# Optimization experiments

Measured on AMD Instinct MI355X. Metric: run time of the kernel, lower is better.

The kernel has to match this reference:

```python
import jax, jax.numpy as jnp
import numpy as np

EPS_NORM = 1e-12  # F.normalize eps
EPS_LN = 1e-5     # nn.LayerNorm default eps

def _l2norm(x, axis=-1):
    n = jnp.linalg.norm(x, axis=axis, keepdims=True)
    return x / jnp.maximum(n, EPS_NORM)

def setup_inputs() -> dict:
    key = jax.random.key(0)
    k1, k2 = jax.random.split(key)
    n, b, d = 2048, 8, 1024
    x = jax.random.normal(k1, (n, b, d), dtype=jnp.float32)
    embed = jax.random.normal(k2, (n, d), dtype=jnp.float32)  # xavier-like
    gamma = jnp.ones((d,), dtype=jnp.float32)
    beta = jnp.zeros((d,), dtype=jnp.float32)
    return {"x": x, "embed": embed, "gamma": gamma, "beta": beta}

def reference(x, embed, gamma, beta):
    # x: [n, b, d]; embed: [n, d] (broadcast over batch, as in .expand)
    wn = _l2norm(embed)          # [n, d]
    xn = _l2norm(x)              # [n, b, d]
    scores = jnp.einsum('nd,mbd->nbm', wn, xn)    # cosine similarities
    weights = jax.nn.softmax(scores, axis=-1)     # [n, b, m]
    out = jnp.einsum('nbm,mbd->nbd', weights, x)  # weighted sum of raw input
    # dropout is identity in eval mode
    y = out + x
    mu = jnp.mean(y, axis=-1, keepdims=True)
    var = jnp.var(y, axis=-1, keepdims=True)
    return (y - mu) * jax.lax.rsqrt(var + EPS_LN) * gamma + beta
```

## Files before the change

### kernel.cpp

```cpp
#include <hip/hip_runtime.h>
#include <hip/hip_bf16.h>

typedef float f4 __attribute__((ext_vector_type(4)));
typedef int i32x4 __attribute__((ext_vector_type(4)));
typedef int i32x8 __attribute__((ext_vector_type(8)));
typedef unsigned char u8x16 __attribute__((ext_vector_type(16)));
typedef unsigned short u16x8 __attribute__((ext_vector_type(8)));

#define N_TOK 2048
#define BATCH 8
#define DIM   1024

#if defined(__has_builtin)
#if __has_builtin(__builtin_amdgcn_cvt_scalef32_pk_fp4_f32)
#define HAS_FP4_CVT 1
#endif
#endif

static __device__ __forceinline__ unsigned char fp8_1(float a) {
  return (unsigned char)(__builtin_amdgcn_cvt_pk_fp8_f32(a, a, 0, false) & 0xFF);
}
static __device__ __forceinline__ unsigned short f2bf(float f) {
  unsigned int b = __float_as_uint(f);
  b += 0x7FFFu + ((b >> 16) & 1u);
  return (unsigned short)(b >> 16);
}
static __device__ __forceinline__ float bf2f(unsigned short u) {
  return __uint_as_float(((unsigned int)u) << 16);
}
static __device__ __forceinline__ unsigned int fp4_enc(float v) {
  const float a = fabsf(v);
  unsigned int c = (a >= 0.25f) + (a >= 0.75f) + (a >= 1.25f) + (a >= 1.75f)
                 + (a >= 2.5f) + (a >= 3.5f) + (a >= 5.0f);
  return c | (v < 0.0f ? 8u : 0u);
}
static __device__ __forceinline__ unsigned int pk8_fp4(const float* v) {
#ifdef HAS_FP4_CVT
  unsigned int r = 0;
  r = __builtin_amdgcn_cvt_scalef32_pk_fp4_f32(r, v[0], v[1], 1.0f, 0);
  r = __builtin_amdgcn_cvt_scalef32_pk_fp4_f32(r, v[2], v[3], 1.0f, 1);
  r = __builtin_amdgcn_cvt_scalef32_pk_fp4_f32(r, v[4], v[5], 1.0f, 2);
  r = __builtin_amdgcn_cvt_scalef32_pk_fp4_f32(r, v[6], v[7], 1.0f, 3);
  return r;
#else
  unsigned int r = 0;
  #pragma unroll
  for (int i = 0; i < 8; ++i) r |= fp4_enc(v[i]) << (i * 4);
  return r;
#endif
}

static __device__ __forceinline__ void gld16(const void* g, void* lds) {
  __builtin_amdgcn_global_load_lds(
      (const __attribute__((address_space(1))) unsigned int*)g,
      (__attribute__((address_space(3))) unsigned int*)lds, 16, 0, 0);
}

static __device__ __forceinline__ void stage_tile(const unsigned char* g, size_t ldb,
                                                  unsigned char* lds, int w, int l) {
  const int rgrp = l >> 3;
  const int srcb = (((l & 7) ^ rgrp) << 4);
  #pragma unroll
  for (int gi = 0; gi < 4; ++gi) {
    int rb = (gi * 4 + w) * 8;
    gld16(g + (size_t)(rb + rgrp) * ldb + srcb, lds + (gi * 4 + w) * 1024);
  }
}

static __device__ __forceinline__ i32x8 fragld32(const unsigned char* lds, int row, int kb) {
  const unsigned char* base = lds + row * 128;
  const int swz = (row & 7) << 4;
  const i32x4 lo = *(const i32x4*)(base + (kb ^ swz));
  const i32x4 hi = *(const i32x4*)(base + ((kb + 16) ^ swz));
  i32x8 r;
  r[0] = lo[0]; r[1] = lo[1]; r[2] = lo[2]; r[3] = lo[3];
  r[4] = hi[0]; r[5] = hi[1]; r[6] = hi[2]; r[7] = hi[3];
  return r;
}
static __device__ __forceinline__ i32x8 fragld16(const unsigned char* lds, int row, int kb) {
  const i32x4 lo = *(const i32x4*)(lds + row * 128 + (kb ^ ((row & 7) << 4)));
  i32x8 r;
  r[0] = lo[0]; r[1] = lo[1]; r[2] = lo[2]; r[3] = lo[3];
  r[4] = 0; r[5] = 0; r[6] = 0; r[7] = 0;
  return r;
}

static __device__ __forceinline__ void gemm_fp4(unsigned char* sA, unsigned char* sB,
    const unsigned char* Ab, size_t lda, const unsigned char* Bb, size_t ldb,
    int nko, int w, int l, int wr, int wc, f4 acc[4][4]) {
  for (int kk = 0; kk < nko; ++kk) {
    stage_tile(Ab + (size_t)kk * 128, lda, sA, w, l);
    stage_tile(Bb + (size_t)kk * 128, ldb, sB, w, l);
    __syncthreads();
    #pragma unroll
    for (int ks = 0; ks < 2; ++ks) {
      const int kb = ks * 64 + (l >> 4) * 16;
      i32x8 af[4], bf[4];
      #pragma unroll
      for (int i = 0; i < 4; ++i)
        af[i] = fragld16(sA, wr * 64 + i * 16 + (l & 15), kb);
      #pragma unroll
      for (int j = 0; j < 4; ++j)
        bf[j] = fragld16(sB, wc * 64 + j * 16 + (l & 15), kb);
      #pragma unroll
      for (int i = 0; i < 4; ++i)
        #pragma unroll
        for (int j = 0; j < 4; ++j)
          acc[i][j] = __builtin_amdgcn_mfma_scale_f32_16x16x128_f8f6f4(
              af[i], bf[j], acc[i][j], 4, 4, 0, 0x7F7F7F7F, 0, 0x7F7F7F7F);
    }
    __syncthreads();
  }
}

static __device__ __forceinline__ void gemm_mixed(unsigned char* sA0, unsigned char* sA1,
    unsigned char* sB, const unsigned char* Ab, size_t lda,
    const unsigned char* Bb, size_t ldb, int nko, int w, int l, int wr, int wc,
    f4 acc[4][4]) {
  for (int kk = 0; kk < nko; ++kk) {
    stage_tile(Ab + (size_t)kk * 256, lda, sA0, w, l);
    stage_tile(Ab + (size_t)kk * 256 + 128, lda, sA1, w, l);
    stage_tile(Bb + (size_t)kk * 128, ldb, sB, w, l);
    __syncthreads();
    #pragma unroll
    for (int ks = 0; ks < 2; ++ks) {
      const unsigned char* sA = ks ? sA1 : sA0;
      const int kbA = (l >> 4) * 32;
      const int kbB = ks * 64 + (l >> 4) * 16;
      i32x8 af[4], bf[4];
      #pragma unroll
      for (int i = 0; i < 4; ++i)
        af[i] = fragld32(sA, wr * 64 + i * 16 + (l & 15), kbA);
      #pragma unroll
      for (int j = 0; j < 4; ++j)
        bf[j] = fragld16(sB, wc * 64 + j * 16 + (l & 15), kbB);
      #pragma unroll
      for (int i = 0; i < 4; ++i)
        #pragma unroll
        for (int j = 0; j < 4; ++j)
          acc[i][j] = __builtin_amdgcn_mfma_scale_f32_16x16x128_f8f6f4(
              af[i], bf[j], acc[i][j], 0, 4, 0, 0x7F7F7F7F, 0, 0x7F7F7F7F);
    }
    __syncthreads();
  }
}


static __device__ __forceinline__ float block_reduce_sum(float v, volatile float* sb, int t) {
  #pragma unroll
  for (int o = 32; o; o >>= 1) v += __shfl_xor(v, o);
  if ((t & 63) == 0) sb[t >> 6] = v;
  __syncthreads();
  float r = sb[0] + sb[1] + sb[2] + sb[3];
  __syncthreads();
  return r;
}

__global__ __launch_bounds__(256) void prep_wn(const float* __restrict__ e,
                                               unsigned char* __restrict__ wn4,
                                               float* __restrict__ winv) {
  __shared__ float sb[4];
  const int n = blockIdx.x, t = threadIdx.x;
  const float4 v = *(const float4*)(e + (size_t)n * DIM + t * 4);
  float ss = v.x * v.x + v.y * v.y + v.z * v.z + v.w * v.w;
  ss = block_reduce_sum(ss, sb, t);
  if (t == 0) winv[n] = rsqrtf(fmaxf(ss, 1e-24f));
  float f[8];
  f[0] = v.x; f[1] = v.y; f[2] = v.z; f[3] = v.w;
  f[4] = 0.0f; f[5] = 0.0f; f[6] = 0.0f; f[7] = 0.0f;
  *(unsigned short*)(wn4 + ((size_t)n * DIM + t * 4) / 2) =
      (unsigned short)(pk8_fp4(f) & 0xFFFFu);
}

template <int XBF>
__global__ __launch_bounds__(256) void prep_x(const float* __restrict__ x,
    unsigned char* __restrict__ xr4, unsigned char* __restrict__ XT4,
    unsigned short* __restrict__ xbf, float* __restrict__ sspart) {
  __shared__ unsigned char tile[64][36];
  const int t = threadIdx.x;
  const int m0 = blockIdx.x * 64, d0 = blockIdx.y * 64, b = blockIdx.z;
  {
    const int ml = t >> 2, dc = (t & 3) * 16;
    const size_t roff = ((size_t)(m0 + ml) * BATCH + b) * DIM + d0 + dc;
    const float* row = x + roff;
    float f[16];
    union { unsigned short u[16]; u16x8 v[2]; } bfp;
    float ssp = 0.0f;
    #pragma unroll
    for (int i = 0; i < 4; ++i) {
      float4 v = *(const float4*)(row + i * 4);
      ssp += v.x * v.x + v.y * v.y + v.z * v.z + v.w * v.w;
      f[i * 4 + 0] = v.x; f[i * 4 + 1] = v.y;
      f[i * 4 + 2] = v.z; f[i * 4 + 3] = v.w;
      if (XBF) {
        bfp.u[i * 4 + 0] = f2bf(v.x); bfp.u[i * 4 + 1] = f2bf(v.y);
        bfp.u[i * 4 + 2] = f2bf(v.z); bfp.u[i * 4 + 3] = f2bf(v.w);
      }
    }
    union { unsigned int u[2]; uint2 v; } pk;
    pk.u[0] = pk8_fp4(f);
    pk.u[1] = pk8_fp4(f + 8);
    *(uint2*)(xr4 + (((size_t)b * N_TOK + m0 + ml) * DIM + d0 + dc) / 2) = pk.v;
    *(unsigned int*)&tile[ml][(t & 3) * 8] = pk.u[0];
    *(unsigned int*)&tile[ml][(t & 3) * 8 + 4] = pk.u[1];
    if (XBF) {
      *(u16x8*)(xbf + roff) = bfp.v[0];
      *(u16x8*)(xbf + roff + 8) = bfp.v[1];
    }
    ssp += __shfl_xor(ssp, 1);
    ssp += __shfl_xor(ssp, 2);
    if ((t & 3) == 0)
      sspart[((size_t)b * N_TOK + m0 + ml) * 16 + (d0 >> 6)] = ssp;
  }
  __syncthreads();
  {
    const int dl = t >> 2, mc = (t & 3) * 16;
    const int sh = (dl & 1) * 4, dby = dl >> 1;
    union { unsigned int u[2]; uint2 v; } o;
    o.u[0] = o.u[1] = 0;
    #pragma unroll
    for (int jj = 0; jj < 8; ++jj) {
      const unsigned int b0 = ((unsigned int)tile[mc + 2 * jj][dby] >> sh) & 15u;
      const unsigned int b1 = ((unsigned int)tile[mc + 2 * jj + 1][dby] >> sh) & 15u;
      o.u[jj >> 2] |= (b0 | (b1 << 4)) << ((jj & 3) * 8);
    }
    *(uint2*)(XT4 + (((size_t)b * DIM + d0 + dl) * (size_t)N_TOK + m0 + mc) / 2) = o.v;
  }
}


__global__ __launch_bounds__(256, 4) void kA(
    const unsigned char* __restrict__ wn4, const unsigned char* __restrict__ xr4,
    const float* __restrict__ winv, const float* __restrict__ sspart,
    unsigned char* __restrict__ Pp, float* __restrict__ pden, int Mc, int c0) {
  __shared__ __align__(16) unsigned char sA[16384];
  __shared__ __align__(16) unsigned char sB[16384];
  __shared__ float pd[128][2];
  __shared__ float winv_s[128], xinv_s[128];

  const int t = threadIdx.x, l = t & 63, w = t >> 6;
  const int wr = w >> 1, wc = w & 1;

  const int gy = Mc >> 7;
  const int nwg = 16 * gy * 8;
  const int lin = blockIdx.x + 16 * (blockIdx.y + gy * blockIdx.z);
  const int wg = (lin & 7) * (nwg >> 3) + (lin >> 3);
  const int xx = wg & 15, yy = (wg >> 4) % gy, zz = (wg >> 4) / gy;

  const int q0 = xx * 128;
  const int m0l = yy * 128;
  const int b = zz;
  const int m0g = c0 + m0l;

  if (t < 128) {
    winv_s[t] = winv[q0 + t];
  } else {
    const float* p = sspart + ((size_t)b * N_TOK + m0g + (t - 128)) * 16;
    float s = 0.0f;
    #pragma unroll
    for (int k = 0; k < 16; ++k) s += p[k];
    xinv_s[t - 128] = rsqrtf(fmaxf(s, 1e-24f));
  }

  f4 acc[4][4];
  #pragma unroll
  for (int i = 0; i < 4; ++i)
    #pragma unroll
    for (int j = 0; j < 4; ++j) acc[i][j] = (f4)0.0f;

  gemm_fp4(sA, sB,
           wn4 + (size_t)q0 * (DIM / 2), DIM / 2,
           xr4 + ((size_t)b * N_TOK + m0g) * (DIM / 2), DIM / 2,
           DIM / 256, w, l, wr, wc, acc);

  float ra[4][4];
  #pragma unroll
  for (int i = 0; i < 4; ++i)
    #pragma unroll
    for (int e = 0; e < 4; ++e) ra[i][e] = 0.0f;

  #pragma unroll
  for (int j = 0; j < 4; ++j) {
    const int cl = wc * 64 + j * 16 + (l & 15);
    const float xv = xinv_s[cl];
    #pragma unroll
    for (int i = 0; i < 4; ++i)
      #pragma unroll
      for (int e = 0; e < 4; ++e) {
        const int row = wr * 64 + i * 16 + (l >> 4) * 4 + e;
        const float p = __expf(acc[i][j][e] * winv_s[row] * xv);
        ra[i][e] += p;
        Pp[((size_t)b * N_TOK + q0 + row) * (size_t)Mc + m0l + cl] = fp8_1(p);
      }
  }
  #pragma unroll
  for (int i = 0; i < 4; ++i)
    #pragma unroll
    for (int e = 0; e < 4; ++e) {
      float s = ra[i][e];
      s += __shfl_xor(s, 1); s += __shfl_xor(s, 2);
      s += __shfl_xor(s, 4); s += __shfl_xor(s, 8);
      if ((l & 15) == 0) pd[wr * 64 + i * 16 + (l >> 4) * 4 + e][wc] = s;
    }
  __syncthreads();
  if (t < 128)
    pden[((size_t)b * N_TOK + q0 + t) * 16 + (c0 >> 7) + yy] = pd[t][0] + pd[t][1];
}


template <int ACC, int FINAL, int OBF>
__global__ __launch_bounds__(256, 3) void kB(const unsigned char* __restrict__ Pp,
    const unsigned char* __restrict__ XT4, const float* __restrict__ pden,
    float* __restrict__ of32, unsigned short* __restrict__ obf, int Mc, int c0) {
  __shared__ __align__(16) unsigned char sA0[16384];
  __shared__ __align__(16) unsigned char sA1[16384];
  __shared__ __align__(16) unsigned char sB[16384];
  __shared__ float rden_s[128];

  const int t = threadIdx.x, l = t & 63, w = t >> 6;
  const int wr = w >> 1, wc = w & 1;

  const int lin = blockIdx.x + 16 * (blockIdx.y + 8 * blockIdx.z);
  const int wg = (lin & 7) * 128 + (lin >> 3);
  const int s = wg & 127;
  const int d0 = (s & 7) * 128;
  const int q0 = (s >> 3) * 128;
  const int b = wg >> 7;

  f4 acc[4][4];
  #pragma unroll
  for (int i = 0; i < 4; ++i)
    #pragma unroll
    for (int j = 0; j < 4; ++j) acc[i][j] = (f4)0.0f;

  gemm_mixed(sA0, sA1, sB,
             Pp + ((size_t)b * N_TOK + q0) * (size_t)Mc, (size_t)Mc,
             XT4 + (((size_t)b * DIM + d0) * (size_t)N_TOK + c0) / 2, N_TOK / 2,
             Mc / 256, w, l, wr, wc, acc);

  if (FINAL) {
    if (t < 128) {
      const float* pp = pden + ((size_t)b * N_TOK + q0 + t) * 16;
      float ss = 0.0f;
      #pragma unroll
      for (int i = 0; i < 16; ++i) ss += pp[i];
      rden_s[t] = 1.0f / ss;
    }
    __syncthreads();
  }

  #pragma unroll
  for (int j = 0; j < 4; ++j) {
    const int cc = d0 + wc * 64 + j * 16 + (l & 15);
    #pragma unroll
    for (int i = 0; i < 4; ++i)
      #pragma unroll
      for (int e = 0; e < 4; ++e) {
        const int rl = wr * 64 + i * 16 + (l >> 4) * 4 + e;
        const size_t oi = (size_t)(q0 + rl) * (BATCH * DIM) + (size_t)b * DIM + cc;
        float v = acc[i][j][e];
        if (ACC) v += of32[oi];
        if (FINAL) {
          v *= rden_s[rl];
          if (OBF) { obf[oi] = f2bf(v); continue; }
        }
        of32[oi] = v;
      }
  }
}


template <int OBF, int XBF>
__global__ __launch_bounds__(256) void kLN(const float* __restrict__ gamma,
    const float* __restrict__ beta, const unsigned short* __restrict__ obf,
    const float* __restrict__ of32, const unsigned short* __restrict__ xbf,
    const float* __restrict__ x, float* __restrict__ out) {
  __shared__ float sb[8];
  const int r = blockIdx.x;
  const int t = threadIdx.x;

  const size_t base = (size_t)r * DIM + t * 4;
  float o0, o1, o2, o3, x0, x1, x2, x3;
  if (OBF) {
    const ushort4 u = *(const ushort4*)(obf + base);
    o0 = bf2f(u.x); o1 = bf2f(u.y); o2 = bf2f(u.z); o3 = bf2f(u.w);
  } else {
    const float4 o4 = *(const float4*)(of32 + base);
    o0 = o4.x; o1 = o4.y; o2 = o4.z; o3 = o4.w;
  }
  if (XBF) {
    const ushort4 u = *(const ushort4*)(xbf + base);
    x0 = bf2f(u.x); x1 = bf2f(u.y); x2 = bf2f(u.z); x3 = bf2f(u.w);
  } else {
    const float4 x4 = *(const float4*)(x + base);
    x0 = x4.x; x1 = x4.y; x2 = x4.z; x3 = x4.w;
  }
  const float y0 = o0 + x0, y1 = o1 + x1, y2 = o2 + x2, y3 = o3 + x3;

  float s1 = y0 + y1 + y2 + y3;
  float s2 = y0 * y0 + y1 * y1 + y2 * y2 + y3 * y3;
  #pragma unroll
  for (int o = 32; o; o >>= 1) { s1 += __shfl_xor(s1, o); s2 += __shfl_xor(s2, o); }
  if ((t & 63) == 0) { sb[t >> 6] = s1; sb[4 + (t >> 6)] = s2; }
  __syncthreads();
  s1 = sb[0] + sb[1] + sb[2] + sb[3];
  s2 = sb[4] + sb[5] + sb[6] + sb[7];

  const float mean = s1 * (1.0f / DIM);
  const float var = s2 * (1.0f / DIM) - mean * mean;
  const float rstd = rsqrtf(var + 1e-5f);

  const float4 g4 = *(const float4*)(gamma + t * 4);
  const float4 b4 = *(const float4*)(beta + t * 4);
  float4 rr;
  rr.x = (y0 - mean) * rstd * g4.x + b4.x;
  rr.y = (y1 - mean) * rstd * g4.y + b4.y;
  rr.z = (y2 - mean) * rstd * g4.z + b4.z;
  rr.w = (y3 - mean) * rstd * g4.w + b4.w;
  *(float4*)(out + (size_t)r * DIM + t * 4) = rr;
}


extern "C" void kernel_launch(void* const* d_in, const int* in_sizes, int n_in,
                              void* d_out, int out_size, void* d_ws, size_t ws_size,
                              hipStream_t stream) {
  (void)in_sizes; (void)n_in; (void)out_size;
  const float* x     = (const float*)d_in[0];
  const float* embed = (const float*)d_in[1];
  const float* gamma = (const float*)d_in[2];
  const float* beta  = (const float*)d_in[3];
  float* out = (float*)d_out;

  size_t off = 0;
  char* ws = (char*)d_ws;
  auto take = [&](size_t bytes) { char* p = ws + off; off += bytes; return p; };
  unsigned char* XT4  = (unsigned char*)take((size_t)BATCH * DIM * N_TOK / 2);
  unsigned char* xr4  = (unsigned char*)take((size_t)BATCH * N_TOK * DIM / 2);
  unsigned char* wn4  = (unsigned char*)take((size_t)N_TOK * DIM / 2);
  float* winv   = (float*)take((size_t)N_TOK * 4);
  float* sspart = (float*)take((size_t)BATCH * N_TOK * 16 * 4);
  float* pden   = (float*)take((size_t)BATCH * N_TOK * 16 * 4);
  const size_t fixed = off;

  int Mc = 2048;
  while (Mc > 256 && fixed + (size_t)BATCH * N_TOK * Mc > ws_size) Mc >>= 1;
  unsigned char* Pp = (unsigned char*)take((size_t)BATCH * N_TOK * Mc);

  const size_t half = (size_t)N_TOK * BATCH * DIM * 2;
  const int use_obf = (off + half <= ws_size) ? 1 : 0;
  unsigned short* obf = use_obf ? (unsigned short*)take(half) : (unsigned short*)out;
  const int use_xbf = (off + half <= ws_size) ? 1 : 0;
  unsigned short* xbf = use_xbf ? (unsigned short*)take(half) : (unsigned short*)out;

  prep_wn<<<N_TOK, 256, 0, stream>>>(embed, wn4, winv);
  if (use_xbf)
    prep_x<1><<<dim3(N_TOK / 64, DIM / 64, BATCH), 256, 0, stream>>>(x, xr4, XT4, xbf, sspart);
  else
    prep_x<0><<<dim3(N_TOK / 64, DIM / 64, BATCH), 256, 0, stream>>>(x, xr4, XT4, xbf, sspart);

  const int nchunk = N_TOK / Mc;
  for (int ci = 0; ci < nchunk; ++ci) {
    const int c0 = ci * Mc;
    kA<<<dim3(16, Mc / 128, BATCH), 256, 0, stream>>>(wn4, xr4, winv, sspart, Pp, pden, Mc, c0);
    const bool first = (ci == 0), last = (ci == nchunk - 1);
    const dim3 gB(16, 8, BATCH);
    if (last) {
      if (use_obf) {
        if (first) kB<0, 1, 1><<<gB, 256, 0, stream>>>(Pp, XT4, pden, out, obf, Mc, c0);
        else       kB<1, 1, 1><<<gB, 256, 0, stream>>>(Pp, XT4, pden, out, obf, Mc, c0);
      } else {
        if (first) kB<0, 1, 0><<<gB, 256, 0, stream>>>(Pp, XT4, pden, out, obf, Mc, c0);
        else       kB<1, 1, 0><<<gB, 256, 0, stream>>>(Pp, XT4, pden, out, obf, Mc, c0);
      }
    } else {
      if (first) kB<0, 0, 0><<<gB, 256, 0, stream>>>(Pp, XT4, pden, out, obf, Mc, c0);
      else       kB<1, 0, 0><<<gB, 256, 0, stream>>>(Pp, XT4, pden, out, obf, Mc, c0);
    }
  }
  if (use_obf) {
    if (use_xbf) kLN<1, 1><<<N_TOK * BATCH, 256, 0, stream>>>(gamma, beta, obf, out, xbf, x, out);
    else         kLN<1, 0><<<N_TOK * BATCH, 256, 0, stream>>>(gamma, beta, obf, out, xbf, x, out);
  } else {
    if (use_xbf) kLN<0, 1><<<N_TOK * BATCH, 256, 0, stream>>>(gamma, beta, obf, out, xbf, x, out);
    else         kLN<0, 0><<<N_TOK * BATCH, 256, 0, stream>>>(gamma, beta, obf, out, xbf, x, out);
  }
}
```

Before: 126.2 us.

## Split x preprocessing into a coalesced row pass and a separate FP4 transpose

```diff
diff --git a/kernel.cpp b/kernel.cpp
--- a/kernel.cpp
+++ b/kernel.cpp
@@ -4,8 +4,7 @@
 typedef float f4 __attribute__((ext_vector_type(4)));
 typedef int i32x4 __attribute__((ext_vector_type(4)));
 typedef int i32x8 __attribute__((ext_vector_type(8)));
-typedef unsigned char u8x16 __attribute__((ext_vector_type(16)));
-typedef unsigned short u16x8 __attribute__((ext_vector_type(8)));
+typedef unsigned short u16x4 __attribute__((ext_vector_type(4)));
 
 #define N_TOK 2048
 #define BATCH 8
@@ -34,19 +33,15 @@
                  + (a >= 2.5f) + (a >= 3.5f) + (a >= 5.0f);
   return c | (v < 0.0f ? 8u : 0u);
 }
-static __device__ __forceinline__ unsigned int pk8_fp4(const float* v) {
+static __device__ __forceinline__ unsigned short pk4_fp4(float a, float b, float c, float d) {
 #ifdef HAS_FP4_CVT
   unsigned int r = 0;
-  r = __builtin_amdgcn_cvt_scalef32_pk_fp4_f32(r, v[0], v[1], 1.0f, 0);
-  r = __builtin_amdgcn_cvt_scalef32_pk_fp4_f32(r, v[2], v[3], 1.0f, 1);
-  r = __builtin_amdgcn_cvt_scalef32_pk_fp4_f32(r, v[4], v[5], 1.0f, 2);
-  r = __builtin_amdgcn_cvt_scalef32_pk_fp4_f32(r, v[6], v[7], 1.0f, 3);
-  return r;
+  r = __builtin_amdgcn_cvt_scalef32_pk_fp4_f32(r, a, b, 1.0f, 0);
+  r = __builtin_amdgcn_cvt_scalef32_pk_fp4_f32(r, c, d, 1.0f, 1);
+  return (unsigned short)(r & 0xFFFFu);
 #else
-  unsigned int r = 0;
-  #pragma unroll
-  for (int i = 0; i < 8; ++i) r |= fp4_enc(v[i]) << (i * 4);
-  return r;
+  return (unsigned short)(fp4_enc(a) | (fp4_enc(b) << 4) |
+                          (fp4_enc(c) << 8) | (fp4_enc(d) << 12));
 #endif
 }
 
@@ -165,52 +160,41 @@
   float ss = v.x * v.x + v.y * v.y + v.z * v.z + v.w * v.w;
   ss = block_reduce_sum(ss, sb, t);
   if (t == 0) winv[n] = rsqrtf(fmaxf(ss, 1e-24f));
-  float f[8];
-  f[0] = v.x; f[1] = v.y; f[2] = v.z; f[3] = v.w;
-  f[4] = 0.0f; f[5] = 0.0f; f[6] = 0.0f; f[7] = 0.0f;
-  *(unsigned short*)(wn4 + ((size_t)n * DIM + t * 4) / 2) =
-      (unsigned short)(pk8_fp4(f) & 0xFFFFu);
+  *(unsigned short*)(wn4 + ((size_t)n * DIM + t * 4) / 2) = pk4_fp4(v.x, v.y, v.z, v.w);
 }
 
 template <int XBF>
-__global__ __launch_bounds__(256) void prep_x(const float* __restrict__ x,
-    unsigned char* __restrict__ xr4, unsigned char* __restrict__ XT4,
-    unsigned short* __restrict__ xbf, float* __restrict__ sspart) {
+__global__ __launch_bounds__(256) void prep_x1(const float* __restrict__ x,
+    unsigned char* __restrict__ xr4, unsigned short* __restrict__ xbf,
+    float* __restrict__ xinv) {
+  __shared__ float sb[4];
+  const int r = blockIdx.x, t = threadIdx.x;
+  const size_t roff = (size_t)r * DIM + t * 4;
+  const float4 v = *(const float4*)(x + roff);
+  float ss = v.x * v.x + v.y * v.y + v.z * v.z + v.w * v.w;
+  ss = block_reduce_sum(ss, sb, t);
+  const int m = r >> 3, b = r & 7;
+  if (t == 0) xinv[b * N_TOK + m] = rsqrtf(fmaxf(ss, 1e-24f));
+  if (XBF) {
+    u16x4 bf;
+    bf[0] = f2bf(v.x); bf[1] = f2bf(v.y); bf[2] = f2bf(v.z); bf[3] = f2bf(v.w);
+    *(u16x4*)(xbf + roff) = bf;
+  }
+  *(unsigned short*)(xr4 + (((size_t)b * N_TOK + m) * DIM + t * 4) / 2) =
+      pk4_fp4(v.x, v.y, v.z, v.w);
+}
+
+__global__ __launch_bounds__(256) void prep_x2(const unsigned char* __restrict__ xr4,
+                                               unsigned char* __restrict__ XT4) {
   __shared__ unsigned char tile[64][36];
   const int t = threadIdx.x;
   const int m0 = blockIdx.x * 64, d0 = blockIdx.y * 64, b = blockIdx.z;
   {
-    const int ml = t >> 2, dc = (t & 3) * 16;
-    const size_t roff = ((size_t)(m0 + ml) * BATCH + b) * DIM + d0 + dc;
-    const float* row = x + roff;
-    float f[16];
-    union { unsigned short u[16]; u16x8 v[2]; } bfp;
-    float ssp = 0.0f;
-    #pragma unroll
-    for (int i = 0; i < 4; ++i) {
-      float4 v = *(const float4*)(row + i * 4);
-      ssp += v.x * v.x + v.y * v.y + v.z * v.z + v.w * v.w;
-      f[i * 4 + 0] = v.x; f[i * 4 + 1] = v.y;
-      f[i * 4 + 2] = v.z; f[i * 4 + 3] = v.w;
-      if (XBF) {
-        bfp.u[i * 4 + 0] = f2bf(v.x); bfp.u[i * 4 + 1] = f2bf(v.y);
-        bfp.u[i * 4 + 2] = f2bf(v.z); bfp.u[i * 4 + 3] = f2bf(v.w);
-      }
-    }
-    union { unsigned int u[2]; uint2 v; } pk;
-    pk.u[0] = pk8_fp4(f);
-    pk.u[1] = pk8_fp4(f + 8);
-    *(uint2*)(xr4 + (((size_t)b * N_TOK + m0 + ml) * DIM + d0 + dc) / 2) = pk.v;
-    *(unsigned int*)&tile[ml][(t & 3) * 8] = pk.u[0];
-    *(unsigned int*)&tile[ml][(t & 3) * 8 + 4] = pk.u[1];
-    if (XBF) {
-      *(u16x8*)(xbf + roff) = bfp.v[0];
-      *(u16x8*)(xbf + roff + 8) = bfp.v[1];
-    }
-    ssp += __shfl_xor(ssp, 1);
-    ssp += __shfl_xor(ssp, 2);
-    if ((t & 3) == 0)
-      sspart[((size_t)b * N_TOK + m0 + ml) * 16 + (d0 >> 6)] = ssp;
+    const int ml = t >> 2, lane = t & 3;
+    const uint2 v = *(const uint2*)(xr4 +
+        (((size_t)b * N_TOK + m0 + ml) * DIM + d0) / 2 + lane * 8);
+    *(unsigned int*)&tile[ml][lane * 8] = v.x;
+    *(unsigned int*)&tile[ml][lane * 8 + 4] = v.y;
   }
   __syncthreads();
   {
@@ -231,7 +215,7 @@
 
 __global__ __launch_bounds__(256, 4) void kA(
     const unsigned char* __restrict__ wn4, const unsigned char* __restrict__ xr4,
-    const float* __restrict__ winv, const float* __restrict__ sspart,
+    const float* __restrict__ winv, const float* __restrict__ xinv,
     unsigned char* __restrict__ Pp, float* __restrict__ pden, int Mc, int c0) {
   __shared__ __align__(16) unsigned char sA[16384];
   __shared__ __align__(16) unsigned char sB[16384];
@@ -252,15 +236,8 @@
   const int b = zz;
   const int m0g = c0 + m0l;
 
-  if (t < 128) {
-    winv_s[t] = winv[q0 + t];
-  } else {
-    const float* p = sspart + ((size_t)b * N_TOK + m0g + (t - 128)) * 16;
-    float s = 0.0f;
-    #pragma unroll
-    for (int k = 0; k < 16; ++k) s += p[k];
-    xinv_s[t - 128] = rsqrtf(fmaxf(s, 1e-24f));
-  }
+  if (t < 128) winv_s[t] = winv[q0 + t];
+  else         xinv_s[t - 128] = xinv[b * N_TOK + m0g + (t - 128)];
 
   f4 acc[4][4];
   #pragma unroll
@@ -438,7 +415,7 @@
   unsigned char* xr4  = (unsigned char*)take((size_t)BATCH * N_TOK * DIM / 2);
   unsigned char* wn4  = (unsigned char*)take((size_t)N_TOK * DIM / 2);
   float* winv   = (float*)take((size_t)N_TOK * 4);
-  float* sspart = (float*)take((size_t)BATCH * N_TOK * 16 * 4);
+  float* xinv   = (float*)take((size_t)BATCH * N_TOK * 4);
   float* pden   = (float*)take((size_t)BATCH * N_TOK * 16 * 4);
   const size_t fixed = off;
 
@@ -454,14 +431,15 @@
 
   prep_wn<<<N_TOK, 256, 0, stream>>>(embed, wn4, winv);
   if (use_xbf)
-    prep_x<1><<<dim3(N_TOK / 64, DIM / 64, BATCH), 256, 0, stream>>>(x, xr4, XT4, xbf, sspart);
+    prep_x1<1><<<N_TOK * BATCH, 256, 0, stream>>>(x, xr4, xbf, xinv);
   else
-    prep_x<0><<<dim3(N_TOK / 64, DIM / 64, BATCH), 256, 0, stream>>>(x, xr4, XT4, xbf, sspart);
+    prep_x1<0><<<N_TOK * BATCH, 256, 0, stream>>>(x, xr4, xbf, xinv);
+  prep_x2<<<dim3(N_TOK / 64, DIM / 64, BATCH), 256, 0, stream>>>(xr4, XT4);
 
   const int nchunk = N_TOK / Mc;
   for (int ci = 0; ci < nchunk; ++ci) {
     const int c0 = ci * Mc;
-    kA<<<dim3(16, Mc / 128, BATCH), 256, 0, stream>>>(wn4, xr4, winv, sspart, Pp, pden, Mc, c0);
+    kA<<<dim3(16, Mc / 128, BATCH), 256, 0, stream>>>(wn4, xr4, winv, xinv, Pp, pden, Mc, c0);
     const bool first = (ci == 0), last = (ci == nchunk - 1);
     const dim3 gB(16, 8, BATCH);
     if (last) {
```

After: 121.3 us. 3.8% less time.
